# Kernel optimization log

Measured on AMD Instinct MI355X. Metric: run time of the kernel, lower is better.

The kernel has to match this reference:

```python
import jax, jax.numpy as jnp
import numpy as np

B, N, D = 128, 512, 512
C = D // 2
K = 4            # topk from init
NUM_SAMPLES = 500
SIGMA = 0.05
NOISE_KEY = jax.random.key(12345)


def perturbed_topk(scores):
    # scores: (B, N) -> indicators (B, K, N)
    b, d = scores.shape
    noise = jax.random.normal(NOISE_KEY, (b, NUM_SAMPLES, d), dtype=scores.dtype)
    perturbed = scores[:, None, :] + noise * SIGMA        # (B, S, N)
    _, idx = jax.lax.top_k(perturbed, K)                  # (B, S, K)
    idx = jnp.sort(idx, axis=-1)
    onehot = jax.nn.one_hot(idx, d, dtype=jnp.float32)    # (B, S, K, N)
    return onehot.mean(axis=1)                            # (B, K, N)


def layer_norm(x, w, b, eps=1e-5):
    mu = x.mean(-1, keepdims=True)
    var = ((x - mu) ** 2).mean(-1, keepdims=True)
    return (x - mu) * jax.lax.rsqrt(var + eps) * w + b


def setup_inputs() -> dict:
    key = jax.random.key(0)
    ks = jax.random.split(key, 8)
    s = lambda fan_in: 1.0 / np.sqrt(fan_in)
    return {
        "x": jax.random.normal(ks[0], (B, N, D), dtype=jnp.float32),
        "input_ids": jax.random.randint(ks[1], (B, N), 0, 30000).astype(jnp.int64),
        "attention_mask": jnp.ones((B, N), dtype=jnp.float32),
        "ln_w": jnp.ones((D,), dtype=jnp.float32),
        "ln_b": jnp.zeros((D,), dtype=jnp.float32),
        "w1": jax.random.uniform(ks[2], (D, C), minval=-s(D), maxval=s(D)),
        "b1": jax.random.uniform(ks[3], (C,), minval=-s(D), maxval=s(D)),
        "w2": jax.random.uniform(ks[4], (D, C), minval=-s(D), maxval=s(D)),
        "w3": jax.random.uniform(ks[5], (C, 1), minval=-s(C), maxval=s(C)),
    }


def reference(x, input_ids, attention_mask, ln_w, ln_b, w1, b1, w2, w3):
    b, n, d = x.shape
    # TextPredictorLG.in_conv: LayerNorm -> Linear(D, D//2) -> GELU (exact erf)
    h = jax.nn.gelu(layer_norm(x, ln_w, ln_b) @ w1 + b1, approximate=False)  # (B,N,C)
    cls_pos = jnp.argmax(input_ids, axis=-1)                                 # (B,)
    g = h[jnp.arange(b), cls_pos][:, None, :]                                # (B,1,C)
    cat = jnp.concatenate([h, jnp.broadcast_to(g, (b, n, C))], axis=-1)      # (B,N,D)
    # out_conv: Linear(D, C, no bias) -> GELU -> Linear(C, 1, no bias) -> Sigmoid
    pred_score = jax.nn.sigmoid(jax.nn.gelu(cat @ w2, approximate=False) @ w3)[..., 0]  # (B,N)
    # shift attention mask left by one, zero-pad last position
    mask_new = jnp.concatenate(
        [attention_mask[:, 1:], jnp.zeros((b, 1), dtype=attention_mask.dtype)], axis=1)
    word_score = pred_score * mask_new                                       # (B,N)
    topk_indicator = perturbed_topk(word_score)                              # (B,K,N)
    cls_x = x[jnp.arange(b), cls_pos][:, None, :]                            # (B,1,D)
    selected = jnp.einsum('bkl,bld->bkd', topk_indicator, x)                 # (B,K,D)
    return jnp.concatenate([cls_x, selected], axis=1)                        # (B,1+K,D)
```

## Files before the change

kernel.cpp:

```cpp
#include <hip/hip_runtime.h>
#include <stdint.h>

#define T_B 128
#define T_N 512
#define T_D 512
#define T_C 256
#define T_S 500
#define T_K 4

#define OFF_HP       0ull
#define OFF_W1HT     67108864ull
#define OFF_W1LT     67371008ull
#define OFF_W2HT     67633152ull
#define OFF_W2LT     67764224ull
#define OFF_ROWSTAT  67895296ull
#define OFF_U        68419584ull
#define OFF_V        68420608ull
#define OFF_GTERM    68421632ull
#define OFF_SCORE    68552704ull
#define OFF_CLSPOS   68814848ull
#define OFF_COUNTS   0ull

typedef __attribute__((ext_vector_type(8))) short bf16x8;
typedef __attribute__((ext_vector_type(4))) float f32x4;

union BF8 { uint32_t u[4]; bf16x8 v; };

__device__ __forceinline__ float gelu_exact(float z) {
  return 0.5f * z * (1.0f + erff(z * 0.70710678118654752440f));
}

__device__ __forceinline__ uint32_t rne_bf16(float f) {
  uint32_t u = __float_as_uint(f);
  return (u + 0x7FFFu + ((u >> 16) & 1u)) >> 16;
}

__device__ __forceinline__ uint2 threefry2x32(uint32_t x0, uint32_t x1) {
  const uint32_t k0 = 0u;
  const uint32_t k1 = 12345u;
  const uint32_t k2 = k0 ^ k1 ^ 0x1BD11BDAu;
  x0 += k0; x1 += k1;
#define TF_ROUND(r) { x0 += x1; x1 = (x1 << (r)) | (x1 >> (32 - (r))); x1 ^= x0; }
  TF_ROUND(13) TF_ROUND(15) TF_ROUND(26) TF_ROUND(6)
  x0 += k1; x1 += k2 + 1u;
  TF_ROUND(17) TF_ROUND(29) TF_ROUND(16) TF_ROUND(24)
  x0 += k2; x1 += k0 + 2u;
  TF_ROUND(13) TF_ROUND(15) TF_ROUND(26) TF_ROUND(6)
  x0 += k0; x1 += k1 + 3u;
  TF_ROUND(17) TF_ROUND(29) TF_ROUND(16) TF_ROUND(24)
  x0 += k1; x1 += k2 + 4u;
  TF_ROUND(13) TF_ROUND(15) TF_ROUND(26) TF_ROUND(6)
  x0 += k2; x1 += k0 + 5u;
#undef TF_ROUND
  return make_uint2(x0, x1);
}

__device__ __forceinline__ void sort4(int a[4]) {
#define CS(x, y) { int lo = min(a[x], a[y]); int hi = max(a[x], a[y]); a[x] = lo; a[y] = hi; }
  CS(0, 1) CS(2, 3) CS(0, 2) CS(1, 3) CS(1, 2)
#undef CS
}


__global__ __launch_bounds__(256) void rowstats_kernel(const float* __restrict__ x,
                                                       float2* __restrict__ rowstat) {
  const int lane = threadIdx.x & 63;
  const int row = blockIdx.x * 4 + (threadIdx.x >> 6);
  const float* xr = x + (size_t)row * 512;
  float vals[8];
  float s = 0.0f;
#pragma unroll
  for (int j = 0; j < 8; j++) { vals[j] = xr[j * 64 + lane]; s += vals[j]; }
#pragma unroll
  for (int m = 1; m < 64; m <<= 1) s += __shfl_xor(s, m);
  const float mu = s * (1.0f / 512.0f);
  float d2 = 0.0f;
#pragma unroll
  for (int j = 0; j < 8; j++) { float d = vals[j] - mu; d2 = fmaf(d, d, d2); }
#pragma unroll
  for (int m = 1; m < 64; m <<= 1) d2 += __shfl_xor(d2, m);
  const float var = d2 * (1.0f / 512.0f);
  if (lane == 0) rowstat[row] = make_float2(mu, rsqrtf(var + 1e-5f));
}

__global__ __launch_bounds__(256) void prep_kernel(const float* __restrict__ w1,
                                                   const float* __restrict__ lnw,
                                                   const float* __restrict__ w2,
                                                   ushort* __restrict__ w1hT,
                                                   ushort* __restrict__ w1lT,
                                                   ushort* __restrict__ w2hT,
                                                   ushort* __restrict__ w2lT) {
  const int c = blockIdx.x;
  const int t = threadIdx.x;
#pragma unroll
  for (int it = 0; it < 2; it++) {
    const int d = t + it * 256;
    const float f = lnw[d] * w1[d * 256 + c];
    const uint32_t hi = rne_bf16(f);
    const float lo = f - __uint_as_float(hi << 16);
    w1hT[c * 512 + d] = (ushort)hi;
    w1lT[c * 512 + d] = (ushort)rne_bf16(lo);
  }
  {
    const float f = w2[t * 256 + c];
    const uint32_t hi = rne_bf16(f);
    const float lo = f - __uint_as_float(hi << 16);
    w2hT[c * 256 + t] = (ushort)hi;
    w2lT[c * 256 + t] = (ushort)rne_bf16(lo);
  }
}

__global__ __launch_bounds__(256) void uv_kernel(const float* __restrict__ w1,
                                                 const float* __restrict__ lnw,
                                                 const float* __restrict__ lnb,
                                                 float* __restrict__ uvec,
                                                 float* __restrict__ vvec) {
  const int c = threadIdx.x;
  float u = 0.0f, v = 0.0f;
  for (int d = 0; d < 512; d++) {
    const float w = w1[d * 256 + c];
    u = fmaf(lnw[d], w, u);
    v = fmaf(lnb[d], w, v);
  }
  uvec[c] = u;
  vvec[c] = v;
}

__global__ __launch_bounds__(64) void clspos_kernel(const int* __restrict__ ids,
                                                    const float* __restrict__ x,
                                                    int* __restrict__ cls_pos,
                                                    float* __restrict__ out) {
  const int b = blockIdx.x;
  const int lane = threadIdx.x;
  unsigned long long best = 0ull;
#pragma unroll
  for (int j = 0; j < 8; j++) {
    const int n = j * 64 + lane;
    const unsigned v = (unsigned)ids[b * 512 + n];
    const unsigned long long key = ((unsigned long long)v << 32) | (unsigned)(511 - n);
    best = key > best ? key : best;
  }
#pragma unroll
  for (int m = 1; m < 64; m <<= 1) {
    const unsigned long long o = __shfl_xor(best, m);
    best = o > best ? o : best;
  }
  const int n = 511 - (int)(best & 0xFFFFFFFFu);
  if (lane == 0) cls_pos[b] = n;
  const float* xr = x + ((size_t)b * 512 + n) * 512;
  float* orow = out + (size_t)b * 2560;
#pragma unroll
  for (int j = 0; j < 8; j++) orow[j * 64 + lane] = xr[j * 64 + lane];
}

__global__ __launch_bounds__(256, 3) void gemm1_mfma(const float* __restrict__ x,
                                                     const ushort* __restrict__ w1hT,
                                                     const ushort* __restrict__ w1lT,
                                                     const float2* __restrict__ rowstat,
                                                     const float* __restrict__ uvec,
                                                     const float* __restrict__ vvec,
                                                     const float* __restrict__ b1,
                                                     uint32_t* __restrict__ Hp) {
  const int l = threadIdx.x & 63;
  const int wid = threadIdx.x >> 6;
  const int wm = wid >> 1, wn = wid & 1;
  const int lr = l & 15;
  const int g  = l >> 4;
  const int row0 = blockIdx.x * 64;

  f32x4 acc[2][8];
#pragma unroll
  for (int mt = 0; mt < 2; mt++)
#pragma unroll
    for (int nt = 0; nt < 8; nt++) acc[mt][nt] = (f32x4)0.0f;

  const float* xb = x + (size_t)(row0 + wm * 32 + lr) * 512 + g * 8;
  const ushort* bhb = w1hT + (size_t)(wn * 128 + lr) * 512 + g * 8;
  const ushort* blb = w1lT + (size_t)(wn * 128 + lr) * 512 + g * 8;

  for (int kt = 0; kt < 16; kt++) {
    const int ko = kt * 32;
    bf16x8 ah[2], al[2];
#pragma unroll
    for (int mt = 0; mt < 2; mt++) {
      const float4 f0 = *(const float4*)(xb + (size_t)mt * 16 * 512 + ko);
      const float4 f1 = *(const float4*)(xb + (size_t)mt * 16 * 512 + ko + 4);
      float f[8] = {f0.x, f0.y, f0.z, f0.w, f1.x, f1.y, f1.z, f1.w};
      BF8 H, L;
#pragma unroll
      for (int p = 0; p < 4; p++) {
        const uint32_t u0 = __float_as_uint(f[2 * p]);
        const uint32_t u1 = __float_as_uint(f[2 * p + 1]);
        H.u[p] = (u0 >> 16) | (u1 & 0xFFFF0000u);
        const float l0 = f[2 * p]     - __uint_as_float(u0 & 0xFFFF0000u);
        const float l1 = f[2 * p + 1] - __uint_as_float(u1 & 0xFFFF0000u);
        L.u[p] = rne_bf16(l0) | (rne_bf16(l1) << 16);
      }
      ah[mt] = H.v; al[mt] = L.v;
    }
#pragma unroll
    for (int nt = 0; nt < 8; nt++) {
      const bf16x8 bh = *(const bf16x8*)(bhb + (size_t)nt * 16 * 512 + ko);
      const bf16x8 bl = *(const bf16x8*)(blb + (size_t)nt * 16 * 512 + ko);
#pragma unroll
      for (int mt = 0; mt < 2; mt++) {
        acc[mt][nt] = __builtin_amdgcn_mfma_f32_16x16x32_bf16(ah[mt], bh, acc[mt][nt], 0, 0, 0);
        acc[mt][nt] = __builtin_amdgcn_mfma_f32_16x16x32_bf16(al[mt], bh, acc[mt][nt], 0, 0, 0);
        acc[mt][nt] = __builtin_amdgcn_mfma_f32_16x16x32_bf16(ah[mt], bl, acc[mt][nt], 0, 0, 0);
      }
    }
  }

#pragma unroll
  for (int mt = 0; mt < 2; mt++) {
    const int Rb = row0 + wm * 32 + mt * 16 + g * 4;
    float2 st[4];
#pragma unroll
    for (int r = 0; r < 4; r++) st[r] = rowstat[Rb + r];
#pragma unroll
    for (int nt = 0; nt < 8; nt++) {
      const int c = wn * 128 + nt * 16 + lr;
      const float uu = uvec[c];
      const float vvb = vvec[c] + b1[c];
      uint32_t pk[4];
#pragma unroll
      for (int r = 0; r < 4; r++) {
        const float z = st[r].y * (acc[mt][nt][r] - st[r].x * uu) + vvb;
        const float gg = gelu_exact(z);
        const uint32_t ug = __float_as_uint(gg);
        const uint32_t hi = ug >> 16;
        const float lo = gg - __uint_as_float(ug & 0xFFFF0000u);
        pk[r] = hi | (rne_bf16(lo) << 16);
      }
      uint32_t* dst = Hp + (size_t)(Rb >> 2) * 1024 + c * 4;
      *(uint4*)dst = make_uint4(pk[0], pk[1], pk[2], pk[3]);
    }
  }
}

__global__ __launch_bounds__(256) void gterm_kernel(const uint32_t* __restrict__ Hp,
                                                    const float* __restrict__ W2,
                                                    const int* __restrict__ cls_pos,
                                                    float* __restrict__ gterm) {
  __shared__ float gsh[256];
  const int b = blockIdx.x;
  const int t = threadIdx.x;
  const int r = b * 512 + cls_pos[b];
  const uint32_t u = Hp[(size_t)(r >> 2) * 1024 + t * 4 + (r & 3)];
  gsh[t] = __uint_as_float((u & 0xFFFFu) << 16) + __uint_as_float(u & 0xFFFF0000u);
  __syncthreads();
  float acc = 0.0f;
  for (int j = 0; j < 256; j++) acc = fmaf(gsh[j], W2[(256 + j) * 256 + t], acc);
  gterm[b * 256 + t] = acc;
}

__global__ __launch_bounds__(256, 3) void gemm2_mfma(const uint32_t* __restrict__ Hp,
                                                     const ushort* __restrict__ w2hT,
                                                     const ushort* __restrict__ w2lT,
                                                     const float* __restrict__ gterm,
                                                     const float* __restrict__ w3,
                                                     const float* __restrict__ amask,
                                                     float* __restrict__ score) {
  __shared__ float sbuf[64][2];
  const int l = threadIdx.x & 63;
  const int wid = threadIdx.x >> 6;
  const int wm = wid >> 1, wn = wid & 1;
  const int lr = l & 15;
  const int g  = l >> 4;
  const int row0 = blockIdx.x * 64;
  const int b = row0 >> 9;

  f32x4 acc[2][8];
#pragma unroll
  for (int mt = 0; mt < 2; mt++)
#pragma unroll
    for (int nt = 0; nt < 8; nt++) acc[mt][nt] = (f32x4)0.0f;

  const uint32_t* ab = Hp + (size_t)(((row0 + wm * 32) >> 2) + (lr >> 2)) * 1024 + (lr & 3) + g * 32;
  const ushort* bhb = w2hT + (size_t)(wn * 128 + lr) * 256 + g * 8;
  const ushort* blb = w2lT + (size_t)(wn * 128 + lr) * 256 + g * 8;

  for (int kt = 0; kt < 8; kt++) {
    const int ko = kt * 32;
    bf16x8 ah[2], al[2];
#pragma unroll
    for (int mt = 0; mt < 2; mt++) {
      const uint32_t* ap = ab + (size_t)mt * 4096 + kt * 128;
      uint32_t u[8];
#pragma unroll
      for (int j = 0; j < 8; j++) u[j] = ap[j * 4];
      BF8 H, L;
#pragma unroll
      for (int p = 0; p < 4; p++) {
        H.u[p] = (u[2 * p] & 0xFFFFu) | (u[2 * p + 1] << 16);
        L.u[p] = (u[2 * p] >> 16) | (u[2 * p + 1] & 0xFFFF0000u);
      }
      ah[mt] = H.v; al[mt] = L.v;
    }
#pragma unroll
    for (int nt = 0; nt < 8; nt++) {
      const bf16x8 bh = *(const bf16x8*)(bhb + (size_t)nt * 16 * 256 + ko);
      const bf16x8 bl = *(const bf16x8*)(blb + (size_t)nt * 16 * 256 + ko);
#pragma unroll
      for (int mt = 0; mt < 2; mt++) {
        acc[mt][nt] = __builtin_amdgcn_mfma_f32_16x16x32_bf16(ah[mt], bh, acc[mt][nt], 0, 0, 0);
        acc[mt][nt] = __builtin_amdgcn_mfma_f32_16x16x32_bf16(al[mt], bh, acc[mt][nt], 0, 0, 0);
        acc[mt][nt] = __builtin_amdgcn_mfma_f32_16x16x32_bf16(ah[mt], bl, acc[mt][nt], 0, 0, 0);
      }
    }
  }

  float s[2][4];
#pragma unroll
  for (int mt = 0; mt < 2; mt++)
#pragma unroll
    for (int r = 0; r < 4; r++) s[mt][r] = 0.0f;

#pragma unroll
  for (int nt = 0; nt < 8; nt++) {
    const int c = wn * 128 + nt * 16 + lr;
    const float gt = gterm[b * 256 + c];
    const float w3v = w3[c];
#pragma unroll
    for (int mt = 0; mt < 2; mt++)
#pragma unroll
      for (int r = 0; r < 4; r++)
        s[mt][r] = fmaf(gelu_exact(acc[mt][nt][r] + gt), w3v, s[mt][r]);
  }
#pragma unroll
  for (int mt = 0; mt < 2; mt++)
#pragma unroll
    for (int r = 0; r < 4; r++) {
#pragma unroll
      for (int m = 1; m < 16; m <<= 1) s[mt][r] += __shfl_xor(s[mt][r], m);
      if (lr == 0) sbuf[wm * 32 + mt * 16 + g * 4 + r][wn] = s[mt][r];
    }
  __syncthreads();
  const int t = threadIdx.x;
  if (t < 64) {
    const float ssum = sbuf[t][0] + sbuf[t][1];
    const int R = row0 + t;
    const int n = R & 511;
    const float mk = (n < 511) ? amask[(R >> 9) * 512 + n + 1] : 0.0f;
    score[R] = mk / (1.0f + expf(-ssum));
  }
}

__global__ __launch_bounds__(256) void topk_kernel(const float* __restrict__ score,
                                                   int* __restrict__ counts) {
  const int lane = threadIdx.x & 63;
  const int wid = threadIdx.x >> 6;
  const int p = blockIdx.x * 4 + wid;
  const int b = p / 500;
  const uint32_t ibase = (uint32_t)p * 512u;
  const float* sc = score + b * 512;

  uint32_t hi[8];
#pragma unroll
  for (int j = 0; j < 8; j++) {
    const int n = (j << 6) + lane;
    const uint2 o = threefry2x32(0u, ibase + (uint32_t)n);
    const uint32_t bits = o.x ^ o.y;
    const float f = __uint_as_float((bits >> 9) | 0x3F800000u) - 1.0f;
    const float x = fmaxf(-0.99999994f, fmaf(f, 2.0f, -0.99999994f));
    const float t = fmaf(-x, x, 1.0f);
    const float w = -0.69314718056f * __log2f(t);
    const float wa = w - 2.5f;
    const float wb = sqrtf(w) - 3.0f;
    float pa = 2.81022636e-08f;
    pa = fmaf(pa, wa, 3.43273939e-07f);
    pa = fmaf(pa, wa, -3.5233877e-06f);
    pa = fmaf(pa, wa, -4.39150654e-06f);
    pa = fmaf(pa, wa, 0.00021858087f);
    pa = fmaf(pa, wa, -0.00125372503f);
    pa = fmaf(pa, wa, -0.00417768164f);
    pa = fmaf(pa, wa, 0.246640727f);
    pa = fmaf(pa, wa, 1.50140941f);
    float pb = -0.000200214257f;
    pb = fmaf(pb, wb, 0.000100950558f);
    pb = fmaf(pb, wb, 0.00134934322f);
    pb = fmaf(pb, wb, -0.00367342844f);
    pb = fmaf(pb, wb, 0.00573950773f);
    pb = fmaf(pb, wb, -0.0076224613f);
    pb = fmaf(pb, wb, 0.00943887047f);
    pb = fmaf(pb, wb, 1.00167406f);
    pb = fmaf(pb, wb, 2.83297682f);
    const float pp = (w < 5.0f) ? pa : pb;
    const float val = fmaf(pp * x, 0.07071067812f, sc[n]);
    hi[j] = __float_as_uint(val + 1.0f);
  }

  int res[4];
#pragma unroll
  for (int it = 0; it < 4; it++) {
    uint32_t bh = hi[0];
    int bl = 511 - lane;
#pragma unroll
    for (int j = 1; j < 8; j++) {
      const int loj = 511 - ((j << 6) + lane);
      if (hi[j] > bh) { bh = hi[j]; bl = loj; }
    }
    unsigned long long k = ((unsigned long long)bh << 32) | (unsigned)bl;
#pragma unroll
    for (int m = 32; m >= 1; m >>= 1) {
      const unsigned long long ok = __shfl_xor(k, m);
      k = ok > k ? ok : k;
    }
    const int bn = 511 - (int)(k & 0xFFFFu);
    res[it] = bn;
    if ((bn & 63) == lane) {
      const int jj = bn >> 6;
#pragma unroll
      for (int j = 0; j < 8; j++)
        if (j == jj) hi[j] = 0u;
    }
  }
  sort4(res);
  if (lane == 0) {
    const int base = b * (T_K * T_N);
#pragma unroll
    for (int kk = 0; kk < 4; kk++)
      atomicAdd(&counts[base + kk * 512 + res[kk]], 1);
  }
}

__global__ __launch_bounds__(256) void select_kernel(const int* __restrict__ counts,
                                                     const float* __restrict__ x,
                                                     float* __restrict__ out) {
  __shared__ float cnt[4][512];
  __shared__ int list[512];
  __shared__ int nlist;
  const int b = blockIdx.x;
  const int t = threadIdx.x;
  if (t == 0) nlist = 0;
  __syncthreads();
  for (int l = t; l < 512; l += 256) {
    const int base = b * 2048 + l;
    const int c0 = counts[base];
    const int c1 = counts[base + 512];
    const int c2 = counts[base + 1024];
    const int c3 = counts[base + 1536];
    cnt[0][l] = (float)c0 * (1.0f / 500.0f);
    cnt[1][l] = (float)c1 * (1.0f / 500.0f);
    cnt[2][l] = (float)c2 * (1.0f / 500.0f);
    cnt[3][l] = (float)c3 * (1.0f / 500.0f);
    if ((c0 | c1 | c2 | c3) != 0) {
      const int pos = atomicAdd(&nlist, 1);
      list[pos] = l;
    }
  }
  __syncthreads();
  const int L = nlist;
  float a0[4] = {0.f, 0.f, 0.f, 0.f};
  float a1[4] = {0.f, 0.f, 0.f, 0.f};
  for (int e = 0; e < L; e++) {
    const int l = list[e];
    const float x0 = x[((size_t)b * 512 + l) * 512 + t];
    const float x1 = x[((size_t)b * 512 + l) * 512 + t + 256];
#pragma unroll
    for (int k = 0; k < 4; k++) {
      const float c = cnt[k][l];
      a0[k] = fmaf(c, x0, a0[k]);
      a1[k] = fmaf(c, x1, a1[k]);
    }
  }
#pragma unroll
  for (int k = 0; k < 4; k++) {
    out[(size_t)b * 2560 + (k + 1) * 512 + t] = a0[k];
    out[(size_t)b * 2560 + (k + 1) * 512 + t + 256] = a1[k];
  }
}

extern "C" void kernel_launch(void* const* d_in, const int* in_sizes, int n_in,
                              void* d_out, int out_size, void* d_ws, size_t ws_size,
                              hipStream_t stream) {
  const float* x     = (const float*)d_in[0];
  const int*   ids   = (const int*)d_in[1];
  const float* amask = (const float*)d_in[2];
  const float* lnw   = (const float*)d_in[3];
  const float* lnb   = (const float*)d_in[4];
  const float* w1    = (const float*)d_in[5];
  const float* b1    = (const float*)d_in[6];
  const float* w2    = (const float*)d_in[7];
  const float* w3    = (const float*)d_in[8];
  float* out = (float*)d_out;
  char* ws = (char*)d_ws;

  uint32_t* Hp     = (uint32_t*)(ws + OFF_HP);
  ushort*   w1hT   = (ushort*)(ws + OFF_W1HT);
  ushort*   w1lT   = (ushort*)(ws + OFF_W1LT);
  ushort*   w2hT   = (ushort*)(ws + OFF_W2HT);
  ushort*   w2lT   = (ushort*)(ws + OFF_W2LT);
  float2*   rowstat= (float2*)(ws + OFF_ROWSTAT);
  float*    uvec   = (float*)(ws + OFF_U);
  float*    vvec   = (float*)(ws + OFF_V);
  float*    gterm  = (float*)(ws + OFF_GTERM);
  float*    score  = (float*)(ws + OFF_SCORE);
  int*      clspos = (int*)(ws + OFF_CLSPOS);
  int*      counts = (int*)(ws + OFF_COUNTS);

  rowstats_kernel<<<16384, 256, 0, stream>>>(x, rowstat);
  prep_kernel<<<256, 256, 0, stream>>>(w1, lnw, w2, w1hT, w1lT, w2hT, w2lT);
  uv_kernel<<<1, 256, 0, stream>>>(w1, lnw, lnb, uvec, vvec);
  clspos_kernel<<<128, 64, 0, stream>>>(ids, x, clspos, out);
  gemm1_mfma<<<1024, 256, 0, stream>>>(x, w1hT, w1lT, rowstat, uvec, vvec, b1, Hp);
  gterm_kernel<<<128, 256, 0, stream>>>(Hp, w2, clspos, gterm);
  gemm2_mfma<<<1024, 256, 0, stream>>>(Hp, w2hT, w2lT, gterm, w3, amask, score);
  hipMemsetAsync(counts, 0, 128 * 4 * 512 * sizeof(int), stream);
  topk_kernel<<<16000, 256, 0, stream>>>(score, counts);
  select_kernel<<<128, 256, 0, stream>>>(counts, x, out);
}
```

Baseline: 668.6 us.

## Stage GEMM tiles through LDS with register prefetch and split column halves

Both MFMA GEMMs now load A and B tiles cooperatively into shared memory, prefetching the next K slice into registers while computing the current one. Each block covers 128 rows by 128 columns, so the grid splits the output columns into two halves and the partial row scores are combined in a new finalize kernel. The Hp layout becomes plain row-major, and the uv reduction is folded into the prep kernel, which removes a single-block launch. The intent is to replace redundant direct global loads with LDS reuse, at the cost of two barriers per K step, possible LDS bank conflicts, and an extra kernel plus a partial-score buffer.

```diff
diff --git a/kernel.cpp b/kernel.cpp
--- a/kernel.cpp
+++ b/kernel.cpp
@@ -19,6 +19,7 @@
 #define OFF_GTERM    68421632ull
 #define OFF_SCORE    68552704ull
 #define OFF_CLSPOS   68814848ull
+#define OFF_SPART    68815360ull
 #define OFF_COUNTS   0ull
 
 typedef __attribute__((ext_vector_type(8))) short bf16x8;
@@ -85,17 +86,25 @@
 
 __global__ __launch_bounds__(256) void prep_kernel(const float* __restrict__ w1,
                                                    const float* __restrict__ lnw,
+                                                   const float* __restrict__ lnb,
                                                    const float* __restrict__ w2,
                                                    ushort* __restrict__ w1hT,
                                                    ushort* __restrict__ w1lT,
                                                    ushort* __restrict__ w2hT,
-                                                   ushort* __restrict__ w2lT) {
+                                                   ushort* __restrict__ w2lT,
+                                                   float* __restrict__ uvec,
+                                                   float* __restrict__ vvec) {
+  __shared__ float redu[4], redv[4];
   const int c = blockIdx.x;
   const int t = threadIdx.x;
+  float usum = 0.0f, vsum = 0.0f;
 #pragma unroll
   for (int it = 0; it < 2; it++) {
     const int d = t + it * 256;
-    const float f = lnw[d] * w1[d * 256 + c];
+    const float wraw = w1[d * 256 + c];
+    const float f = lnw[d] * wraw;
+    usum += f;
+    vsum = fmaf(lnb[d], wraw, vsum);
     const uint32_t hi = rne_bf16(f);
     const float lo = f - __uint_as_float(hi << 16);
     w1hT[c * 512 + d] = (ushort)hi;
@@ -108,22 +117,17 @@
     w2hT[c * 256 + t] = (ushort)hi;
     w2lT[c * 256 + t] = (ushort)rne_bf16(lo);
   }
-}
-
-__global__ __launch_bounds__(256) void uv_kernel(const float* __restrict__ w1,
-                                                 const float* __restrict__ lnw,
-                                                 const float* __restrict__ lnb,
-                                                 float* __restrict__ uvec,
-                                                 float* __restrict__ vvec) {
-  const int c = threadIdx.x;
-  float u = 0.0f, v = 0.0f;
-  for (int d = 0; d < 512; d++) {
-    const float w = w1[d * 256 + c];
-    u = fmaf(lnw[d], w, u);
-    v = fmaf(lnb[d], w, v);
-  }
-  uvec[c] = u;
-  vvec[c] = v;
+#pragma unroll
+  for (int m = 1; m < 64; m <<= 1) {
+    usum += __shfl_xor(usum, m);
+    vsum += __shfl_xor(vsum, m);
+  }
+  if ((t & 63) == 0) { redu[t >> 6] = usum; redv[t >> 6] = vsum; }
+  __syncthreads();
+  if (t == 0) {
+    uvec[c] = redu[0] + redu[1] + redu[2] + redu[3];
+    vvec[c] = redv[0] + redv[1] + redv[2] + redv[3];
+  }
 }
 
 __global__ __launch_bounds__(64) void clspos_kernel(const int* __restrict__ ids,
@@ -153,20 +157,37 @@
   for (int j = 0; j < 8; j++) orow[j * 64 + lane] = xr[j * 64 + lane];
 }
 
-__global__ __launch_bounds__(256, 3) void gemm1_mfma(const float* __restrict__ x,
-                                                     const ushort* __restrict__ w1hT,
-                                                     const ushort* __restrict__ w1lT,
-                                                     const float2* __restrict__ rowstat,
-                                                     const float* __restrict__ uvec,
-                                                     const float* __restrict__ vvec,
-                                                     const float* __restrict__ b1,
-                                                     uint32_t* __restrict__ Hp) {
-  const int l = threadIdx.x & 63;
-  const int wid = threadIdx.x >> 6;
-  const int wm = wid >> 1, wn = wid & 1;
-  const int lr = l & 15;
-  const int g  = l >> 4;
-  const int row0 = blockIdx.x * 64;
+__global__ __launch_bounds__(256) void gemm1_p(const float* __restrict__ x,
+                                               const ushort* __restrict__ w1hT,
+                                               const ushort* __restrict__ w1lT,
+                                               const float2* __restrict__ rowstat,
+                                               const float* __restrict__ uvec,
+                                               const float* __restrict__ vvec,
+                                               const float* __restrict__ b1,
+                                               uint32_t* __restrict__ Hp) {
+  __shared__ float  As[128][32];
+  __shared__ ushort Bs[2][128][32];
+  const int t = threadIdx.x;
+  const int lane = t & 63;
+  const int wm = t >> 6;
+  const int lr = lane & 15;
+  const int g  = lane >> 4;
+  const int bx = blockIdx.x;
+  const int row0 = (bx >> 1) * 128;
+  const int col0 = (bx & 1) * 128;
+
+  const float*  ax  = x    + (size_t)(row0 + (t >> 3)) * 512 + (t & 7) * 4;
+  const ushort* bh0 = w1hT + (size_t)(col0 + (t >> 2)) * 512 + (t & 3) * 8;
+  const ushort* bl0 = w1lT + (size_t)(col0 + (t >> 2)) * 512 + (t & 3) * 8;
+
+  uint4 ra[4], rb[4];
+#pragma unroll
+  for (int i = 0; i < 4; i++) ra[i] = *(const uint4*)(ax + (size_t)i * 32 * 512);
+#pragma unroll
+  for (int i = 0; i < 2; i++) {
+    rb[i]     = *(const uint4*)(bh0 + (size_t)i * 64 * 512);
+    rb[2 + i] = *(const uint4*)(bl0 + (size_t)i * 64 * 512);
+  }
 
   f32x4 acc[2][8];
 #pragma unroll
@@ -174,17 +195,34 @@
 #pragma unroll
     for (int nt = 0; nt < 8; nt++) acc[mt][nt] = (f32x4)0.0f;
 
-  const float* xb = x + (size_t)(row0 + wm * 32 + lr) * 512 + g * 8;
-  const ushort* bhb = w1hT + (size_t)(wn * 128 + lr) * 512 + g * 8;
-  const ushort* blb = w1lT + (size_t)(wn * 128 + lr) * 512 + g * 8;
-
+  uint32_t* const Ab = (uint32_t*)&As[0][0];
+  uint32_t* const Bb = (uint32_t*)&Bs[0][0][0];
+
+#pragma unroll 1
   for (int kt = 0; kt < 16; kt++) {
-    const int ko = kt * 32;
+#pragma unroll
+    for (int i = 0; i < 4; i++) *(uint4*)(Ab + i * 1024 + t * 4) = ra[i];
+#pragma unroll
+    for (int i = 0; i < 2; i++) {
+      *(uint4*)(Bb + i * 1024 + t * 4)        = rb[i];
+      *(uint4*)(Bb + 2048 + i * 1024 + t * 4) = rb[2 + i];
+    }
+    __syncthreads();
+    if (kt < 15) {
+      const int ko = (kt + 1) * 32;
+#pragma unroll
+      for (int i = 0; i < 4; i++) ra[i] = *(const uint4*)(ax + (size_t)i * 32 * 512 + ko);
+#pragma unroll
+      for (int i = 0; i < 2; i++) {
+        rb[i]     = *(const uint4*)(bh0 + (size_t)i * 64 * 512 + ko);
+        rb[2 + i] = *(const uint4*)(bl0 + (size_t)i * 64 * 512 + ko);
+      }
+    }
     bf16x8 ah[2], al[2];
 #pragma unroll
     for (int mt = 0; mt < 2; mt++) {
-      const float4 f0 = *(const float4*)(xb + (size_t)mt * 16 * 512 + ko);
-      const float4 f1 = *(const float4*)(xb + (size_t)mt * 16 * 512 + ko + 4);
+      const float4 f0 = *(const float4*)&As[wm * 32 + mt * 16 + lr][g * 8];
+      const float4 f1 = *(const float4*)&As[wm * 32 + mt * 16 + lr][g * 8 + 4];
       float f[8] = {f0.x, f0.y, f0.z, f0.w, f1.x, f1.y, f1.z, f1.w};
       BF8 H, L;
 #pragma unroll
@@ -200,8 +238,8 @@
     }
 #pragma unroll
     for (int nt = 0; nt < 8; nt++) {
-      const bf16x8 bh = *(const bf16x8*)(bhb + (size_t)nt * 16 * 512 + ko);
-      const bf16x8 bl = *(const bf16x8*)(blb + (size_t)nt * 16 * 512 + ko);
+      const bf16x8 bh = *(const bf16x8*)&Bs[0][nt * 16 + lr][g * 8];
+      const bf16x8 bl = *(const bf16x8*)&Bs[1][nt * 16 + lr][g * 8];
 #pragma unroll
       for (int mt = 0; mt < 2; mt++) {
         acc[mt][nt] = __builtin_amdgcn_mfma_f32_16x16x32_bf16(ah[mt], bh, acc[mt][nt], 0, 0, 0);
@@ -209,6 +247,7 @@
         acc[mt][nt] = __builtin_amdgcn_mfma_f32_16x16x32_bf16(ah[mt], bl, acc[mt][nt], 0, 0, 0);
       }
     }
+    __syncthreads();
   }
 
 #pragma unroll
@@ -219,10 +258,9 @@
     for (int r = 0; r < 4; r++) st[r] = rowstat[Rb + r];
 #pragma unroll
     for (int nt = 0; nt < 8; nt++) {
-      const int c = wn * 128 + nt * 16 + lr;
+      const int c = col0 + nt * 16 + lr;
       const float uu = uvec[c];
       const float vvb = vvec[c] + b1[c];
-      uint32_t pk[4];
 #pragma unroll
       for (int r = 0; r < 4; r++) {
         const float z = st[r].y * (acc[mt][nt][r] - st[r].x * uu) + vvb;
@@ -230,10 +268,8 @@
         const uint32_t ug = __float_as_uint(gg);
         const uint32_t hi = ug >> 16;
         const float lo = gg - __uint_as_float(ug & 0xFFFF0000u);
-        pk[r] = hi | (rne_bf16(lo) << 16);
-      }
-      uint32_t* dst = Hp + (size_t)(Rb >> 2) * 1024 + c * 4;
-      *(uint4*)dst = make_uint4(pk[0], pk[1], pk[2], pk[3]);
+        Hp[(size_t)(Rb + r) * 256 + c] = hi | (rne_bf16(lo) << 16);
+      }
     }
   }
 }
@@ -246,7 +282,7 @@
   const int b = blockIdx.x;
   const int t = threadIdx.x;
   const int r = b * 512 + cls_pos[b];
-  const uint32_t u = Hp[(size_t)(r >> 2) * 1024 + t * 4 + (r & 3)];
+  const uint32_t u = Hp[(size_t)r * 256 + t];
   gsh[t] = __uint_as_float((u & 0xFFFFu) << 16) + __uint_as_float(u & 0xFFFF0000u);
   __syncthreads();
   float acc = 0.0f;
@@ -254,41 +290,72 @@
   gterm[b * 256 + t] = acc;
 }
 
-__global__ __launch_bounds__(256, 3) void gemm2_mfma(const uint32_t* __restrict__ Hp,
-                                                     const ushort* __restrict__ w2hT,
-                                                     const ushort* __restrict__ w2lT,
-                                                     const float* __restrict__ gterm,
-                                                     const float* __restrict__ w3,
-                                                     const float* __restrict__ amask,
-                                                     float* __restrict__ score) {
-  __shared__ float sbuf[64][2];
-  const int l = threadIdx.x & 63;
-  const int wid = threadIdx.x >> 6;
-  const int wm = wid >> 1, wn = wid & 1;
-  const int lr = l & 15;
-  const int g  = l >> 4;
-  const int row0 = blockIdx.x * 64;
+__global__ __launch_bounds__(256) void gemm2_p(const uint32_t* __restrict__ Hp,
+                                               const ushort* __restrict__ w2hT,
+                                               const ushort* __restrict__ w2lT,
+                                               const float* __restrict__ gterm,
+                                               const float* __restrict__ w3,
+                                               float* __restrict__ spart) {
+  __shared__ uint32_t As[128][32];
+  __shared__ ushort   Bs[2][128][32];
+  const int t = threadIdx.x;
+  const int lane = t & 63;
+  const int wm = t >> 6;
+  const int lr = lane & 15;
+  const int g  = lane >> 4;
+  const int bx = blockIdx.x;
+  const int row0 = (bx >> 1) * 128;
+  const int col0 = (bx & 1) * 128;
   const int b = row0 >> 9;
 
+  const uint32_t* axp = Hp   + (size_t)(row0 + (t >> 3)) * 256 + (t & 7) * 4;
+  const ushort*   bh0 = w2hT + (size_t)(col0 + (t >> 2)) * 256 + (t & 3) * 8;
+  const ushort*   bl0 = w2lT + (size_t)(col0 + (t >> 2)) * 256 + (t & 3) * 8;
+
+  uint4 ra[4], rb[4];
+#pragma unroll
+  for (int i = 0; i < 4; i++) ra[i] = *(const uint4*)(axp + (size_t)i * 32 * 256);
+#pragma unroll
+  for (int i = 0; i < 2; i++) {
+    rb[i]     = *(const uint4*)(bh0 + (size_t)i * 64 * 256);
+    rb[2 + i] = *(const uint4*)(bl0 + (size_t)i * 64 * 256);
+  }
+
   f32x4 acc[2][8];
 #pragma unroll
   for (int mt = 0; mt < 2; mt++)
 #pragma unroll
     for (int nt = 0; nt < 8; nt++) acc[mt][nt] = (f32x4)0.0f;
 
-  const uint32_t* ab = Hp + (size_t)(((row0 + wm * 32) >> 2) + (lr >> 2)) * 1024 + (lr & 3) + g * 32;
-  const ushort* bhb = w2hT + (size_t)(wn * 128 + lr) * 256 + g * 8;
-  const ushort* blb = w2lT + (size_t)(wn * 128 + lr) * 256 + g * 8;
-
+  uint32_t* const Ab = (uint32_t*)&As[0][0];
+  uint32_t* const Bb = (uint32_t*)&Bs[0][0][0];
+
+#pragma unroll 1
   for (int kt = 0; kt < 8; kt++) {
-    const int ko = kt * 32;
+#pragma unroll
+    for (int i = 0; i < 4; i++) *(uint4*)(Ab + i * 1024 + t * 4) = ra[i];
+#pragma unroll
+    for (int i = 0; i < 2; i++) {
+      *(uint4*)(Bb + i * 1024 + t * 4)        = rb[i];
+      *(uint4*)(Bb + 2048 + i * 1024 + t * 4) = rb[2 + i];
+    }
+    __syncthreads();
+    if (kt < 7) {
+      const int ko = (kt + 1) * 32;
+#pragma unroll
+      for (int i = 0; i < 4; i++) ra[i] = *(const uint4*)(axp + (size_t)i * 32 * 256 + ko);
+#pragma unroll
+      for (int i = 0; i < 2; i++) {
+        rb[i]     = *(const uint4*)(bh0 + (size_t)i * 64 * 256 + ko);
+        rb[2 + i] = *(const uint4*)(bl0 + (size_t)i * 64 * 256 + ko);
+      }
+    }
     bf16x8 ah[2], al[2];
 #pragma unroll
     for (int mt = 0; mt < 2; mt++) {
-      const uint32_t* ap = ab + (size_t)mt * 4096 + kt * 128;
-      uint32_t u[8];
-#pragma unroll
-      for (int j = 0; j < 8; j++) u[j] = ap[j * 4];
+      const uint4 q0 = *(const uint4*)&As[wm * 32 + mt * 16 + lr][g * 8];
+      const uint4 q1 = *(const uint4*)&As[wm * 32 + mt * 16 + lr][g * 8 + 4];
+      const uint32_t u[8] = {q0.x, q0.y, q0.z, q0.w, q1.x, q1.y, q1.z, q1.w};
       BF8 H, L;
 #pragma unroll
       for (int p = 0; p < 4; p++) {
@@ -299,8 +366,8 @@
     }
 #pragma unroll
     for (int nt = 0; nt < 8; nt++) {
-      const bf16x8 bh = *(const bf16x8*)(bhb + (size_t)nt * 16 * 256 + ko);
-      const bf16x8 bl = *(const bf16x8*)(blb + (size_t)nt * 16 * 256 + ko);
+      const bf16x8 bh = *(const bf16x8*)&Bs[0][nt * 16 + lr][g * 8];
+      const bf16x8 bl = *(const bf16x8*)&Bs[1][nt * 16 + lr][g * 8];
 #pragma unroll
       for (int mt = 0; mt < 2; mt++) {
         acc[mt][nt] = __builtin_amdgcn_mfma_f32_16x16x32_bf16(ah[mt], bh, acc[mt][nt], 0, 0, 0);
@@ -308,6 +375,7 @@
         acc[mt][nt] = __builtin_amdgcn_mfma_f32_16x16x32_bf16(ah[mt], bl, acc[mt][nt], 0, 0, 0);
       }
     }
+    __syncthreads();
   }
 
   float s[2][4];
@@ -315,10 +383,9 @@
   for (int mt = 0; mt < 2; mt++)
 #pragma unroll
     for (int r = 0; r < 4; r++) s[mt][r] = 0.0f;
-
 #pragma unroll
   for (int nt = 0; nt < 8; nt++) {
-    const int c = wn * 128 + nt * 16 + lr;
+    const int c = col0 + nt * 16 + lr;
     const float gt = gterm[b * 256 + c];
     const float w3v = w3[c];
 #pragma unroll
@@ -333,17 +400,21 @@
     for (int r = 0; r < 4; r++) {
 #pragma unroll
       for (int m = 1; m < 16; m <<= 1) s[mt][r] += __shfl_xor(s[mt][r], m);
-      if (lr == 0) sbuf[wm * 32 + mt * 16 + g * 4 + r][wn] = s[mt][r];
-    }
-  __syncthreads();
-  const int t = threadIdx.x;
-  if (t < 64) {
-    const float ssum = sbuf[t][0] + sbuf[t][1];
-    const int R = row0 + t;
-    const int n = R & 511;
-    const float mk = (n < 511) ? amask[(R >> 9) * 512 + n + 1] : 0.0f;
-    score[R] = mk / (1.0f + expf(-ssum));
-  }
+      if (lr == 0) {
+        const int R = row0 + wm * 32 + mt * 16 + g * 4 + r;
+        spart[(bx & 1) * 65536 + R] = s[mt][r];
+      }
+    }
+}
+
+__global__ __launch_bounds__(256) void finalize_kernel(const float* __restrict__ spart,
+                                                       const float* __restrict__ amask,
+                                                       float* __restrict__ score) {
+  const int r = blockIdx.x * 256 + threadIdx.x;
+  const float ssum = spart[r] + spart[65536 + r];
+  const int n = r & 511;
+  const float mk = (n < 511) ? amask[(r >> 9) * 512 + n + 1] : 0.0f;
+  score[r] = mk / (1.0f + expf(-ssum));
 }
 
 __global__ __launch_bounds__(256) void topk_kernel(const float* __restrict__ score,
@@ -497,15 +568,16 @@
   float*    gterm  = (float*)(ws + OFF_GTERM);
   float*    score  = (float*)(ws + OFF_SCORE);
   int*      clspos = (int*)(ws + OFF_CLSPOS);
+  float*    spart  = (float*)(ws + OFF_SPART);
   int*      counts = (int*)(ws + OFF_COUNTS);
 
   rowstats_kernel<<<16384, 256, 0, stream>>>(x, rowstat);
-  prep_kernel<<<256, 256, 0, stream>>>(w1, lnw, w2, w1hT, w1lT, w2hT, w2lT);
-  uv_kernel<<<1, 256, 0, stream>>>(w1, lnw, lnb, uvec, vvec);
+  prep_kernel<<<256, 256, 0, stream>>>(w1, lnw, lnb, w2, w1hT, w1lT, w2hT, w2lT, uvec, vvec);
   clspos_kernel<<<128, 64, 0, stream>>>(ids, x, clspos, out);
-  gemm1_mfma<<<1024, 256, 0, stream>>>(x, w1hT, w1lT, rowstat, uvec, vvec, b1, Hp);
+  gemm1_p<<<1024, 256, 0, stream>>>(x, w1hT, w1lT, rowstat, uvec, vvec, b1, Hp);
   gterm_kernel<<<128, 256, 0, stream>>>(Hp, w2, clspos, gterm);
-  gemm2_mfma<<<1024, 256, 0, stream>>>(Hp, w2hT, w2lT, gterm, w3, amask, score);
+  gemm2_p<<<1024, 256, 0, stream>>>(Hp, w2hT, w2lT, gterm, w3, spart);
+  finalize_kernel<<<256, 256, 0, stream>>>(spart, amask, score);
   hipMemsetAsync(counts, 0, 128 * 4 * 512 * sizeof(int), stream);
   topk_kernel<<<16000, 256, 0, stream>>>(score, counts);
   select_kernel<<<128, 256, 0, stream>>>(counts, x, out);
```

Result: no change. 672.3 us (+0.6%).
